# Performance work log

Measured on AMD Instinct MI355X. Metric: run time of the kernel, lower is better.

## Reference

```python
import jax, jax.numpy as jnp
import numpy as np

EPS = 1e-5  # torch BatchNorm2d default eps
B, C, H, W, G = 32, 256, 56, 56, 32


def setup_inputs() -> dict:
    key = jax.random.key(0)
    ks = jax.random.split(key, 12)
    x = jax.random.normal(ks[0], (B, C, H, W), dtype=jnp.float32)
    labels = jax.random.randint(ks[1], (B,), 0, 1000)
    # alpha_net: Conv2d(C, 1, 1) -> weight [1,C,1,1] flattened to [C], bias [1]
    alpha_w = jax.random.normal(ks[2], (C,), dtype=jnp.float32) * 0.05
    alpha_b = jnp.zeros((1,), dtype=jnp.float32)
    # global BatchNorm2d (eval mode: affine + running stats)
    g_w = 1.0 + 0.1 * jax.random.normal(ks[3], (C,), dtype=jnp.float32)
    g_b = 0.1 * jax.random.normal(ks[4], (C,), dtype=jnp.float32)
    g_rm = 0.1 * jax.random.normal(ks[5], (C,), dtype=jnp.float32)
    g_rv = 0.5 + jax.random.uniform(ks[6], (C,), dtype=jnp.float32)
    # per-group BatchNorm2d params, stacked [G, C]
    grp_w = 1.0 + 0.1 * jax.random.normal(ks[7], (G, C), dtype=jnp.float32)
    grp_b = 0.1 * jax.random.normal(ks[8], (G, C), dtype=jnp.float32)
    grp_rm = 0.1 * jax.random.normal(ks[9], (G, C), dtype=jnp.float32)
    grp_rv = 0.5 + jax.random.uniform(ks[10], (G, C), dtype=jnp.float32)
    return {"x": x, "labels": labels, "alpha_w": alpha_w, "alpha_b": alpha_b,
            "g_w": g_w, "g_b": g_b, "g_rm": g_rm, "g_rv": g_rv,
            "grp_w": grp_w, "grp_b": grp_b, "grp_rm": grp_rm, "grp_rv": grp_rv}


def reference(x, labels, alpha_w, alpha_b, g_w, g_b, g_rm, g_rv,
              grp_w, grp_b, grp_rm, grp_rv):
    # alpha gate: global avg pool -> 1x1 conv (C->1) -> sigmoid, per-sample scalar
    pooled = x.mean(axis=(2, 3))                       # [B, C]
    alpha = jax.nn.sigmoid(pooled @ alpha_w + alpha_b[0])  # [B]
    alpha = alpha[:, None, None, None]                 # [B,1,1,1]

    # global BN (eval): per-channel affine from running stats
    gs = g_w * jax.lax.rsqrt(g_rv + EPS)               # [C]
    gsh = g_b - g_rm * gs                              # [C]
    x_global = x * gs[None, :, None, None] + gsh[None, :, None, None]

    # eval path: mean over all G group BNs == single mean scale/shift per channel
    sg = grp_w * jax.lax.rsqrt(grp_rv + EPS)           # [G, C]
    ms = sg.mean(axis=0)                               # [C]
    msh = (grp_b - grp_rm * sg).mean(axis=0)           # [C]
    x_groups = x * ms[None, :, None, None] + msh[None, :, None, None]

    return (1.0 - alpha) * x_global + alpha * x_groups
```

## Files before the change

### kernel.cpp

```cpp
#include <hip/hip_runtime.h>
#include <math.h>

#define B_ 32
#define C_ 256
#define HW_ 3136
#define HW4_ 784
#define G_ 32
#define EPS_ 1e-5f

__global__ __launch_bounds__(256) void pool_kernel(const float* __restrict__ x,
                                                   float* __restrict__ pooled) {
    const int bc = blockIdx.x;
    const float4* __restrict__ p = (const float4*)(x + (size_t)bc * HW_);
    const int tid = threadIdx.x;
    float s = 0.f;
    for (int i = tid; i < HW4_; i += 256) {
        float4 v = p[i];
        s += v.x + v.y + v.z + v.w;
    }
    #pragma unroll
    for (int off = 32; off; off >>= 1) s += __shfl_down(s, off);
    __shared__ float red[4];
    const int lane = tid & 63, wv = tid >> 6;
    if (lane == 0) red[wv] = s;
    __syncthreads();
    if (tid == 0) {
        float t = red[0] + red[1] + red[2] + red[3];
        pooled[bc] = t * (1.f / HW_);
    }
}

__global__ __launch_bounds__(256) void alpha_scale_kernel(
    const float* __restrict__ pooled,
    const float* __restrict__ alpha_w, const float* __restrict__ alpha_b,
    const float* __restrict__ g_w, const float* __restrict__ g_b,
    const float* __restrict__ g_rm, const float* __restrict__ g_rv,
    const float* __restrict__ grp_w, const float* __restrict__ grp_b,
    const float* __restrict__ grp_rm, const float* __restrict__ grp_rv,
    float* __restrict__ scale, float* __restrict__ shift) {
    const int b = blockIdx.x;
    const int c = threadIdx.x;
    float s = pooled[b * C_ + c] * alpha_w[c];
    #pragma unroll
    for (int off = 32; off; off >>= 1) s += __shfl_down(s, off);
    __shared__ float red[4];
    __shared__ float alpha_sh;
    const int lane = c & 63, wv = c >> 6;
    if (lane == 0) red[wv] = s;
    __syncthreads();
    if (c == 0) {
        float z = red[0] + red[1] + red[2] + red[3] + alpha_b[0];
        alpha_sh = 1.f / (1.f + expf(-z));
    }
    __syncthreads();
    const float a = alpha_sh;

    float gs  = g_w[c] * rsqrtf(g_rv[c] + EPS_);
    float gsh = g_b[c] - g_rm[c] * gs;
    float mss = 0.f, mshs = 0.f;
    #pragma unroll 8
    for (int g = 0; g < G_; ++g) {
        float sg = grp_w[g * C_ + c] * rsqrtf(grp_rv[g * C_ + c] + EPS_);
        mss  += sg;
        mshs += grp_b[g * C_ + c] - grp_rm[g * C_ + c] * sg;
    }
    float ms  = mss  * (1.f / G_);
    float msh = mshs * (1.f / G_);

    scale[b * C_ + c] = (1.f - a) * gs  + a * ms;
    shift[b * C_ + c] = (1.f - a) * gsh + a * msh;
}

__global__ __launch_bounds__(256) void apply_kernel(const float* __restrict__ x,
                                                    const float* __restrict__ scale,
                                                    const float* __restrict__ shift,
                                                    float* __restrict__ out) {
    const int bc = blockIdx.x;
    const float sc = scale[bc];
    const float sh = shift[bc];
    const float4* __restrict__ px = (const float4*)(x + (size_t)bc * HW_);
    float4* __restrict__ po = (float4*)(out + (size_t)bc * HW_);
    for (int i = threadIdx.x; i < HW4_; i += 256) {
        float4 v = px[i];
        float4 r;
        r.x = fmaf(v.x, sc, sh);
        r.y = fmaf(v.y, sc, sh);
        r.z = fmaf(v.z, sc, sh);
        r.w = fmaf(v.w, sc, sh);
        po[i] = r;
    }
}

extern "C" void kernel_launch(void* const* d_in, const int* in_sizes, int n_in,
                              void* d_out, int out_size, void* d_ws, size_t ws_size,
                              hipStream_t stream) {
    const float* x       = (const float*)d_in[0];
    const float* alpha_w = (const float*)d_in[2];
    const float* alpha_b = (const float*)d_in[3];
    const float* g_w     = (const float*)d_in[4];
    const float* g_b     = (const float*)d_in[5];
    const float* g_rm    = (const float*)d_in[6];
    const float* g_rv    = (const float*)d_in[7];
    const float* grp_w   = (const float*)d_in[8];
    const float* grp_b   = (const float*)d_in[9];
    const float* grp_rm  = (const float*)d_in[10];
    const float* grp_rv  = (const float*)d_in[11];
    float* out = (float*)d_out;

    float* pooled = (float*)d_ws;
    float* scale  = pooled + B_ * C_;
    float* shift  = scale  + B_ * C_;

    pool_kernel<<<B_ * C_, 256, 0, stream>>>(x, pooled);
    alpha_scale_kernel<<<B_, 256, 0, stream>>>(pooled, alpha_w, alpha_b,
                                               g_w, g_b, g_rm, g_rv,
                                               grp_w, grp_b, grp_rm, grp_rv,
                                               scale, shift);
    apply_kernel<<<B_ * C_, 256, 0, stream>>>(x, scale, shift, out);
}
```

Before: 219.0 us.

## Fold alpha/BN parameter kernel into pool and apply kernels, use atomics and nontemporal stores

Removes the middle alpha_scale kernel. The pool kernel now atomically accumulates the alpha dot product per sample, and batch-0 blocks precompute the per-channel BN scales and shifts. The apply kernel computes the sigmoid and the blended scale and shift per block, and writes its output with nontemporal stores. This saves one launch and the serialized small kernel, at the cost of a memset, atomic contention (256 adds per sample), and an extra launch for the memset.

After: 273.7 us. +24.9%, slower.

```diff
diff --git a/kernel.cpp b/kernel.cpp
--- a/kernel.cpp
+++ b/kernel.cpp
@@ -8,11 +8,26 @@
 #define G_ 32
 #define EPS_ 1e-5f
 
-__global__ __launch_bounds__(256) void pool_kernel(const float* __restrict__ x,
-                                                   float* __restrict__ pooled) {
+#define WS_ALPHA 0
+#define WS_GS    32
+#define WS_GSH   (32 + 256)
+#define WS_MS    (32 + 512)
+#define WS_MSH   (32 + 768)
+
+__global__ __launch_bounds__(256) void pool_fold_kernel(
+    const float* __restrict__ x,
+    const float* __restrict__ alpha_w,
+    const float* __restrict__ g_w, const float* __restrict__ g_b,
+    const float* __restrict__ g_rm, const float* __restrict__ g_rv,
+    const float* __restrict__ grp_w, const float* __restrict__ grp_b,
+    const float* __restrict__ grp_rm, const float* __restrict__ grp_rv,
+    float* __restrict__ ws) {
     const int bc = blockIdx.x;
+    const int c  = bc & (C_ - 1);
+    const int b  = bc >> 8;
+    const int tid = threadIdx.x;
+
     const float4* __restrict__ p = (const float4*)(x + (size_t)bc * HW_);
-    const int tid = threadIdx.x;
     float s = 0.f;
     for (int i = tid; i < HW4_; i += 256) {
         float4 v = p[i];
@@ -25,59 +40,45 @@
     if (lane == 0) red[wv] = s;
     __syncthreads();
     if (tid == 0) {
-        float t = red[0] + red[1] + red[2] + red[3];
-        pooled[bc] = t * (1.f / HW_);
+        float mean = (red[0] + red[1] + red[2] + red[3]) * (1.f / HW_);
+        atomicAdd(ws + WS_ALPHA + b, mean * alpha_w[c]);
+    }
+
+    if (b == 0 && tid < G_) {
+        const int g = tid;
+        float sg = grp_w[g * C_ + c] * rsqrtf(grp_rv[g * C_ + c] + EPS_);
+        float sh = grp_b[g * C_ + c] - grp_rm[g * C_ + c] * sg;
+        #pragma unroll
+        for (int off = 16; off; off >>= 1) {
+            sg += __shfl_down(sg, off);
+            sh += __shfl_down(sh, off);
+        }
+        if (g == 0) {
+            ws[WS_MS  + c] = sg * (1.f / G_);
+            ws[WS_MSH + c] = sh * (1.f / G_);
+            float gsv = g_w[c] * rsqrtf(g_rv[c] + EPS_);
+            ws[WS_GS  + c] = gsv;
+            ws[WS_GSH + c] = g_b[c] - g_rm[c] * gsv;
+        }
     }
 }
 
-__global__ __launch_bounds__(256) void alpha_scale_kernel(
-    const float* __restrict__ pooled,
-    const float* __restrict__ alpha_w, const float* __restrict__ alpha_b,
-    const float* __restrict__ g_w, const float* __restrict__ g_b,
-    const float* __restrict__ g_rm, const float* __restrict__ g_rv,
-    const float* __restrict__ grp_w, const float* __restrict__ grp_b,
-    const float* __restrict__ grp_rm, const float* __restrict__ grp_rv,
-    float* __restrict__ scale, float* __restrict__ shift) {
-    const int b = blockIdx.x;
-    const int c = threadIdx.x;
-    float s = pooled[b * C_ + c] * alpha_w[c];
-    #pragma unroll
-    for (int off = 32; off; off >>= 1) s += __shfl_down(s, off);
-    __shared__ float red[4];
-    __shared__ float alpha_sh;
-    const int lane = c & 63, wv = c >> 6;
-    if (lane == 0) red[wv] = s;
-    __syncthreads();
-    if (c == 0) {
-        float z = red[0] + red[1] + red[2] + red[3] + alpha_b[0];
-        alpha_sh = 1.f / (1.f + expf(-z));
-    }
-    __syncthreads();
-    const float a = alpha_sh;
+__global__ __launch_bounds__(256) void apply_kernel(
+    const float* __restrict__ x,
+    const float* __restrict__ ws,
+    const float* __restrict__ alpha_b,
+    float* __restrict__ out) {
+    const int bc = blockIdx.x;
+    const int c  = bc & (C_ - 1);
+    const int b  = bc >> 8;
 
-    float gs  = g_w[c] * rsqrtf(g_rv[c] + EPS_);
-    float gsh = g_b[c] - g_rm[c] * gs;
-    float mss = 0.f, mshs = 0.f;
-    #pragma unroll 8
-    for (int g = 0; g < G_; ++g) {
-        float sg = grp_w[g * C_ + c] * rsqrtf(grp_rv[g * C_ + c] + EPS_);
-        mss  += sg;
-        mshs += grp_b[g * C_ + c] - grp_rm[g * C_ + c] * sg;
-    }
-    float ms  = mss  * (1.f / G_);
-    float msh = mshs * (1.f / G_);
+    float z  = ws[WS_ALPHA + b] + alpha_b[0];
+    float a  = 1.f / (1.f + __expf(-z));
+    float gs  = ws[WS_GS  + c], gsh = ws[WS_GSH + c];
+    float ms  = ws[WS_MS  + c], msh = ws[WS_MSH + c];
+    const float sc = fmaf(a, ms - gs, gs);
+    const float sh = fmaf(a, msh - gsh, gsh);
 
-    scale[b * C_ + c] = (1.f - a) * gs  + a * ms;
-    shift[b * C_ + c] = (1.f - a) * gsh + a * msh;
-}
-
-__global__ __launch_bounds__(256) void apply_kernel(const float* __restrict__ x,
-                                                    const float* __restrict__ scale,
-                                                    const float* __restrict__ shift,
-                                                    float* __restrict__ out) {
-    const int bc = blockIdx.x;
-    const float sc = scale[bc];
-    const float sh = shift[bc];
     const float4* __restrict__ px = (const float4*)(x + (size_t)bc * HW_);
     float4* __restrict__ po = (float4*)(out + (size_t)bc * HW_);
     for (int i = threadIdx.x; i < HW4_; i += 256) {
@@ -87,7 +88,10 @@
         r.y = fmaf(v.y, sc, sh);
         r.z = fmaf(v.z, sc, sh);
         r.w = fmaf(v.w, sc, sh);
-        po[i] = r;
+        __builtin_nontemporal_store(r.x, &po[i].x);
+        __builtin_nontemporal_store(r.y, &po[i].y);
+        __builtin_nontemporal_store(r.z, &po[i].z);
+        __builtin_nontemporal_store(r.w, &po[i].w);
     }
 }
 
@@ -106,15 +110,13 @@
     const float* grp_rm  = (const float*)d_in[10];
     const float* grp_rv  = (const float*)d_in[11];
     float* out = (float*)d_out;
+    float* ws  = (float*)d_ws;
 
-    float* pooled = (float*)d_ws;
-    float* scale  = pooled + B_ * C_;
-    float* shift  = scale  + B_ * C_;
+    hipMemsetAsync(ws, 0, B_ * sizeof(float), stream);
 
-    pool_kernel<<<B_ * C_, 256, 0, stream>>>(x, pooled);
-    alpha_scale_kernel<<<B_, 256, 0, stream>>>(pooled, alpha_w, alpha_b,
-                                               g_w, g_b, g_rm, g_rv,
-                                               grp_w, grp_b, grp_rm, grp_rv,
-                                               scale, shift);
-    apply_kernel<<<B_ * C_, 256, 0, stream>>>(x, scale, shift, out);
+    pool_fold_kernel<<<B_ * C_, 256, 0, stream>>>(x, alpha_w,
+                                                  g_w, g_b, g_rm, g_rv,
+                                                  grp_w, grp_b, grp_rm, grp_rv,
+                                                  ws);
+    apply_kernel<<<B_ * C_, 256, 0, stream>>>(x, ws, alpha_b, out);
 }
```
